# Performance work log

Measured on AMD Instinct MI355X. Metric: run time of the kernel, lower is better.

Reference implementation:

```python
import jax, jax.numpy as jnp
import numpy as np

N = 100000      # nodes
E = 1600000     # edges (before self loops)
H = 64          # hidden channels (per-head out dim, concat=False)
HEADS = 2
L = 2           # num GAT blocks
IN = 64
OUT = 10
B = 64          # graphs in batch
SLOPE = 0.2     # LeakyReLU negative slope (GATv2Conv default)
EPS = 1e-5      # BatchNorm eps


def setup_inputs() -> dict:
    key = jax.random.key(0)
    ks = jax.random.split(key, 10)
    s = 0.05
    x = jax.random.normal(ks[0], (N, IN), jnp.float32)
    edge_index = jax.random.randint(ks[1], (2, E), 0, N, dtype=jnp.int64)
    batch = jnp.sort(jax.random.randint(ks[2], (N,), 0, B, dtype=jnp.int64))
    W_enc = jax.random.normal(ks[3], (IN, H), jnp.float32) * s
    b_enc = jnp.zeros((H,), jnp.float32)
    Wl = jax.random.normal(ks[4], (L, H, HEADS * H), jnp.float32) * s
    bl = jnp.zeros((L, HEADS * H), jnp.float32)
    Wr = jax.random.normal(ks[5], (L, H, HEADS * H), jnp.float32) * s
    br = jnp.zeros((L, HEADS * H), jnp.float32)
    att = jax.random.normal(ks[6], (L, HEADS, H), jnp.float32) * s
    bias = jnp.zeros((L, H), jnp.float32)
    gamma = jnp.ones((L, H), jnp.float32)
    beta = jnp.zeros((L, H), jnp.float32)
    W_cls = jax.random.normal(ks[7], (H, OUT), jnp.float32) * s
    b_cls = jnp.zeros((OUT,), jnp.float32)
    return dict(x=x, edge_index=edge_index, batch=batch, W_enc=W_enc, b_enc=b_enc,
                Wl=Wl, bl=bl, Wr=Wr, br=br, att=att, bias=bias,
                gamma=gamma, beta=beta, W_cls=W_cls, b_cls=b_cls)


def reference(x, edge_index, batch, W_enc, b_enc, Wl, bl, Wr, br, att, bias,
              gamma, beta, W_cls, b_cls):
    # add self loops (GATv2Conv default add_self_loops=True)
    loops = jnp.arange(N, dtype=edge_index.dtype)
    ei = jnp.concatenate([edge_index, jnp.stack([loops, loops])], axis=1)
    src, dst = ei[0], ei[1]

    h = x @ W_enc + b_enc                                   # [N, H] atom encoder (Linear)
    for l in range(L):
        xl = (h @ Wl[l] + bl[l]).reshape(N, HEADS, H)       # source transform
        xr = (h @ Wr[l] + br[l]).reshape(N, HEADS, H)       # target transform
        # GATv2: e_uv = a^T LeakyReLU(W_l x_u + W_r x_v)
        z = jax.nn.leaky_relu(xl[src] + xr[dst], SLOPE)     # [E', heads, H]
        e = jnp.einsum('ehc,hc->eh', z, att[l])             # [E', heads]
        # segment softmax over incoming edges of each dst node
        m = jax.ops.segment_max(e, dst, num_segments=N)     # [N, heads]
        ex = jnp.exp(e - m[dst])
        den = jax.ops.segment_sum(ex, dst, num_segments=N)
        alpha = ex / den[dst]                               # [E', heads]
        out = jax.ops.segment_sum(xl[src] * alpha[:, :, None], dst, num_segments=N)
        h_new = out.mean(axis=1) + bias[l]                  # concat=False: mean over heads
        # BatchNorm1d (batch statistics) -> ReLU; dropout=0
        mu = h_new.mean(axis=0)
        var = h_new.var(axis=0)
        h = jax.nn.relu((h_new - mu) * jax.lax.rsqrt(var + EPS) * gamma[l] + beta[l])

    # global mean pool over graphs
    cnt = jax.ops.segment_sum(jnp.ones((N,), h.dtype), batch, num_segments=B)
    g = jax.ops.segment_sum(h, batch, num_segments=B) / jnp.maximum(cnt, 1.0)[:, None]
    return g @ W_cls + b_cls                                # [B, OUT]
```

## Files before the change

### kernel.cpp

```cpp
#include <hip/hip_runtime.h>

#define N_NODES 100000
#define E_EDGES 1600000
#define EP_EDGES (E_EDGES + N_NODES)
#define SLOPE 0.2f
#define BN_EPS 1e-5f
#define NB 8
#define NODES_PER_B 12500
#define NREP 32
#define SUBREG 8192
#define SCATTER_BLKS ((EP_EDGES + 255) / 256)

typedef _Float16 h2 __attribute__((ext_vector_type(2)));

#if defined(__has_builtin)
#if __has_builtin(__builtin_amdgcn_fdot2)
#define HAVE_FDOT2 1
#endif
#endif

__device__ __forceinline__ float fdot2f(h2 a, h2 b, float c) {
#ifdef HAVE_FDOT2
    return __builtin_amdgcn_fdot2(a, b, c, false);
#else
    return c + (float)a[0] * (float)b[0] + (float)a[1] * (float)b[1];
#endif
}
__device__ __forceinline__ h2 bch2(unsigned u) { return __builtin_bit_cast(h2, u); }
__device__ __forceinline__ h2 habs2(h2 z) {
    return __builtin_bit_cast(h2, (unsigned)(__builtin_bit_cast(unsigned, z) & 0x7fff7fffu));
}
__device__ __forceinline__ h2 shflx_h2(h2 a, int o) {
    return __builtin_bit_cast(h2, __shfl_xor(__builtin_bit_cast(int, a), o, 64));
}

template <int CTRL>
__device__ __forceinline__ float dpp_add_step(float v) {
    int r = __builtin_amdgcn_update_dpp(0, __float_as_int(v), CTRL, 0xF, 0xF, false);
    return v + __int_as_float(r);
}
__device__ __forceinline__ float rowsum16(float v) {
    v = dpp_add_step<0x128>(v);
    v = dpp_add_step<0x124>(v);
    v = dpp_add_step<0x122>(v);
    v = dpp_add_step<0x121>(v);
    return v;
}

__device__ __forceinline__ void bucket_scatter_body(int bid, const int* __restrict__ src,
                                                    const int* __restrict__ dst,
                                                    int* __restrict__ gcur, unsigned* __restrict__ ebuf) {
    int i = bid * 256 + threadIdx.x;
    int rep = bid & (NREP - 1);
    bool active = i < EP_EDGES;
    int s = 0, d = 0;
    if (i < E_EDGES) { s = src[i]; d = dst[i]; }
    else if (active) { s = i - E_EDGES; d = s; }
    int b = active ? (int)((unsigned)d / NODES_PER_B) : NB;
    unsigned long long lt = (1ull << (threadIdx.x & 63)) - 1ull;
    int rank = 0;
    unsigned long long mymask = 0;
#pragma unroll
    for (int bb = 0; bb < NB; ++bb) {
        unsigned long long m = __ballot(b == bb);
        if (b == bb) { rank = __popcll(m & lt); mymask = m; }
    }
    int leader = mymask ? (__ffsll((long long)mymask) - 1) : 0;
    int lanebit = threadIdx.x & 63;
    int chunkbase = 0;
    if (active && lanebit == leader)
        chunkbase = atomicAdd(&gcur[rep * NB + b], (int)__popcll(mymask));
    chunkbase = __shfl(chunkbase, leader, 64);
    if (active) {
        unsigned dl = (unsigned)d - (unsigned)b * NODES_PER_B;
        ebuf[(size_t)(rep * NB + b) * SUBREG + chunkbase + rank] = (dl << 17) | (unsigned)s;
    }
}

__device__ __forceinline__ void fuse_enc_body(const float* __restrict__ We, const float* __restrict__ be,
                                              const float* __restrict__ Wl, const float* __restrict__ bl,
                                              const float* __restrict__ Wr, const float* __restrict__ br,
                                              float* __restrict__ Wcl, float* __restrict__ bcl,
                                              float* __restrict__ Wcr, float* __restrict__ bcr,
                                              float (*sWe)[64], float* sbe) {
    int t = threadIdx.x;
    for (int i = t; i < 4096; i += 256) sWe[i & 63][i >> 6] = We[i];
    if (t < 64) sbe[t] = be[t];
    __syncthreads();
    int j = t & 127, side = t >> 7;
    const float* W  = side ? Wr : Wl;
    const float* bb = side ? br : bl;
    float acc[64];
#pragma unroll
    for (int k = 0; k < 64; ++k) acc[k] = 0.f;
    float bacc = bb[j];
    for (int m = 0; m < 64; ++m) {
        float wv = W[m * 128 + j];
        bacc += sbe[m] * wv;
#pragma unroll
        for (int k = 0; k < 64; ++k) acc[k] += sWe[m][k] * wv;
    }
    float* Wc = side ? Wcr : Wcl;
#pragma unroll
    for (int k = 0; k < 64; ++k) Wc[k * 128 + j] = acc[k];
    (side ? bcr : bcl)[j] = bacc;
}

__global__ __launch_bounds__(256) void scatter_fuse(const int* __restrict__ src, const int* __restrict__ dst,
                                                    int* __restrict__ gcur, unsigned* __restrict__ ebuf,
                                                    const float* __restrict__ We, const float* __restrict__ be,
                                                    const float* __restrict__ Wl, const float* __restrict__ bl,
                                                    const float* __restrict__ Wr, const float* __restrict__ br,
                                                    float* __restrict__ Wcl, float* __restrict__ bcl,
                                                    float* __restrict__ Wcr, float* __restrict__ bcr) {
    __shared__ float sWe[64][64];
    __shared__ float sbe[64];
    if (blockIdx.x == 0)
        fuse_enc_body(We, be, Wl, bl, Wr, br, Wcl, bcl, Wcr, bcr, sWe, sbe);
    else
        bucket_scatter_body(blockIdx.x - 1, src, dst, gcur, ebuf);
}

__global__ __launch_bounds__(256) void bucket_deg(const int* __restrict__ gcur,
                                                  const unsigned* __restrict__ ebuf,
                                                  int* __restrict__ deg) {
    __shared__ int ldeg[NODES_PER_B];
    int b = blockIdx.x & (NB - 1), rep = blockIdx.x >> 3;
    for (int j = threadIdx.x; j < NODES_PER_B; j += 256) ldeg[j] = 0;
    __syncthreads();
    int cnt = gcur[rep * NB + b];
    int base = b * NODES_PER_B;
    const unsigned* p = ebuf + (size_t)(rep * NB + b) * SUBREG;
    for (int i = threadIdx.x; i < cnt; i += 256)
        atomicAdd(&ldeg[p[i] >> 17], 1);
    __syncthreads();
    for (int j = threadIdx.x; j < NODES_PER_B; j += 256) {
        int v = ldeg[j];
        if (v) atomicAdd(&deg[base + j], v);
    }
}

__device__ __forceinline__ void bucket_fine_body(int bid, const int* __restrict__ gcur,
                                                 const unsigned* __restrict__ ebuf,
                                                 int* __restrict__ cursor, int* __restrict__ col) {
    int b = bid & (NB - 1), rep = bid >> 3;
    int cnt = gcur[rep * NB + b];
    int base = b * NODES_PER_B;
    const unsigned* p = ebuf + (size_t)(rep * NB + b) * SUBREG;
    for (int i = threadIdx.x; i < cnt; i += 256) {
        unsigned e = p[i];
        int d = base + (int)(e >> 17), s = (int)(e & 0x1FFFFu);
        int pos = atomicAdd(&cursor[d], 1);
        col[pos] = s;
    }
}

__global__ void scan_a(const int* __restrict__ deg, int* __restrict__ row_ptr, int* __restrict__ bsum) {
    __shared__ int wsum[16];
    int tid = threadIdx.x;
    int lane = tid & 63;
    int i = blockIdx.x * 1024 + tid;
    int x = (i < N_NODES) ? deg[i] : 0;
#pragma unroll
    for (int o = 1; o < 64; o <<= 1) {
        int y = __shfl_up(x, o, 64);
        if (lane >= o) x += y;
    }
    if (lane == 63) wsum[tid >> 6] = x;
    __syncthreads();
    if (tid < 16) {
        int s = wsum[tid];
#pragma unroll
        for (int o = 1; o < 16; o <<= 1) {
            int y = __shfl_up(s, o, 16);
            if (tid >= o) s += y;
        }
        wsum[tid] = s;
    }
    __syncthreads();
    int pre = (tid >= 64) ? wsum[(tid >> 6) - 1] : 0;
    int incl = x + pre;
    if (i < N_NODES) row_ptr[i + 1] = incl;
    if (tid == 1023) bsum[blockIdx.x] = incl;
}

__global__ void scan_c(int* __restrict__ cursor, int* __restrict__ row_ptr, const int* __restrict__ bsum) {
    __shared__ int sp[128];
    int t = threadIdx.x;
    if (t < 128) sp[t] = (t < 98) ? bsum[t] : 0;
    __syncthreads();
    for (int o = 1; o < 128; o <<= 1) {
        int v = (t < 128 && t >= o) ? sp[t - o] : 0;
        __syncthreads();
        if (t < 128) sp[t] += v;
        __syncthreads();
    }
    int i = blockIdx.x * 256 + t;
    if (i < N_NODES) {
        int d = cursor[i];
        int blk = i >> 10;
        int pre = blk ? sp[blk - 1] : 0;
        int incl = row_ptr[i + 1] + pre;
        row_ptr[i + 1] = incl;
        cursor[i] = incl - d;
        if (i == 0) row_ptr[0] = 0;
    }
}

template <int BN>
__device__ __forceinline__ void layer_gemm_body(int bid, int nb,
                                                const float* __restrict__ hin,
                                                const float* __restrict__ Wl, const float* __restrict__ bl,
                                                const float* __restrict__ Wr, const float* __restrict__ br,
                                                const float* __restrict__ bns, const float* __restrict__ gamma,
                                                const float* __restrict__ beta,
                                                unsigned short* __restrict__ xl, unsigned short* __restrict__ xr,
                                                float* ssc, float* ssh, h2 (*sh)[36]) {
    int t = threadIdx.x;
    if (BN) {
        if (t < 64) {
            float s = 0.f, sq = 0.f;
#pragma unroll
            for (int r = 0; r < 8; ++r) { s += bns[r * 128 + t]; sq += bns[r * 128 + 64 + t]; }
            float mu = s * (1.f / N_NODES);
            float var = sq * (1.f / N_NODES) - mu * mu;
            float sc = gamma[t] * rsqrtf(var + BN_EPS);
            ssc[t] = sc; ssh[t] = beta[t] - mu * sc;
        }
        __syncthreads();
    }
    int p = t & 127, rh = t >> 7;
    int col0 = 2 * p;
    bool isR = col0 >= 128;
    int cw0 = col0 & 127, cw1 = cw0 + 1;
    const float* W = isR ? Wr : Wl;
    h2 w2a[32], w2b[32];
#pragma unroll
    for (int k2 = 0; k2 < 32; ++k2) {
        w2a[k2] = (h2){(_Float16)W[(2 * k2) * 128 + cw0], (_Float16)W[(2 * k2 + 1) * 128 + cw0]};
        w2b[k2] = (h2){(_Float16)W[(2 * k2) * 128 + cw1], (_Float16)W[(2 * k2 + 1) * 128 + cw1]};
    }
    float bja = (isR ? br : bl)[cw0];
    float bjb = (isR ? br : bl)[cw1];
    int head0 = cw0 >> 6, c0 = cw0 & 63;
    int head1 = cw1 >> 6, c1 = cw1 & 63;
    int oidx0 = ((c0 >> 2) << 3) + (head0 << 2) + (c0 & 3);
    int oidx1 = ((c1 >> 2) << 3) + (head1 << 2) + (c1 & 3);
    unsigned short* dstp = isR ? xr : xl;
    for (int base = bid * 16; base < N_NODES; base += nb * 16) {
        __syncthreads();
#pragma unroll
        for (int pass = 0; pass < 2; ++pass) {
            int i = t + pass * 256;
            int node = i >> 5, pr = i & 31;
            int gnode = base + node;
            int cc = pr * 2;
            float2 v = make_float2(0.f, 0.f);
            if (gnode < N_NODES) v = *(const float2*)(hin + (size_t)gnode * 64 + cc);
            if (BN) {
                v.x = fmaxf(v.x * ssc[cc] + ssh[cc], 0.f);
                v.y = fmaxf(v.y * ssc[cc + 1] + ssh[cc + 1], 0.f);
            }
            sh[node][pr] = (h2){(_Float16)v.x, (_Float16)v.y};
        }
        __syncthreads();
        int lim = min(16, N_NODES - base);
        int rend = min(rh * 8 + 8, lim);
        for (int r = rh * 8; r < rend; ++r) {
            float acca = bja, accb = bjb;
            const uint4* r4 = (const uint4*)(&sh[r][0]);
#pragma unroll
            for (int k4 = 0; k4 < 8; ++k4) {
                uint4 u = r4[k4];
                acca = fdot2f(bch2(u.x), w2a[4 * k4 + 0], acca);
                accb = fdot2f(bch2(u.x), w2b[4 * k4 + 0], accb);
                acca = fdot2f(bch2(u.y), w2a[4 * k4 + 1], acca);
                accb = fdot2f(bch2(u.y), w2b[4 * k4 + 1], accb);
                acca = fdot2f(bch2(u.z), w2a[4 * k4 + 2], acca);
                accb = fdot2f(bch2(u.z), w2b[4 * k4 + 2], accb);
                acca = fdot2f(bch2(u.w), w2a[4 * k4 + 3], acca);
                accb = fdot2f(bch2(u.w), w2b[4 * k4 + 3], accb);
            }
            size_t rowb = (size_t)(base + r) * 128;
            dstp[rowb + oidx0] = __builtin_bit_cast(unsigned short, (_Float16)acca);
            dstp[rowb + oidx1] = __builtin_bit_cast(unsigned short, (_Float16)accb);
        }
    }
}

__global__ __launch_bounds__(256) void fine_gemm0(const int* __restrict__ gcur,
                                                  const unsigned* __restrict__ ebuf,
                                                  int* __restrict__ cursor, int* __restrict__ col,
                                                  const float* __restrict__ hin,
                                                  const float* __restrict__ Wl, const float* __restrict__ bl,
                                                  const float* __restrict__ Wr, const float* __restrict__ br,
                                                  unsigned short* __restrict__ xl, unsigned short* __restrict__ xr) {
    __shared__ float ssc[64], ssh[64];
    __shared__ h2 sh[16][36];
    if (blockIdx.x < NREP * NB)
        bucket_fine_body(blockIdx.x, gcur, ebuf, cursor, col);
    else
        layer_gemm_body<0>(blockIdx.x - NREP * NB, 1024, hin, Wl, bl, Wr, br,
                           nullptr, nullptr, nullptr, xl, xr, ssc, ssh, sh);
}

__global__ __launch_bounds__(256) void layer_gemm1(const float* __restrict__ hin,
                                                   const float* __restrict__ Wl, const float* __restrict__ bl,
                                                   const float* __restrict__ Wr, const float* __restrict__ br,
                                                   const float* __restrict__ bns, const float* __restrict__ gamma,
                                                   const float* __restrict__ beta,
                                                   unsigned short* __restrict__ xl, unsigned short* __restrict__ xr) {
    __shared__ float ssc[64], ssh[64];
    __shared__ h2 sh[16][36];
    layer_gemm_body<1>(blockIdx.x, gridDim.x, hin, Wl, bl, Wr, br, bns, gamma, beta, xl, xr, ssc, ssh, sh);
}

__global__ __launch_bounds__(256) void aggregate(const char* __restrict__ xlb,
                                                 const uint4* __restrict__ xr4,
                                                 const int* __restrict__ row_ptr, const int* __restrict__ col,
                                                 const float* __restrict__ att_l, const float* __restrict__ bias_l,
                                                 float* __restrict__ hn, float* __restrict__ bnsum) {
    int lane = threadIdx.x & 63, wid = threadIdx.x >> 6;
    int q = lane >> 4, k = lane & 15;
    int koff = k << 4;
    h2 atA0 = {(_Float16)att_l[4 * k], (_Float16)att_l[4 * k + 1]};
    h2 atA1 = {(_Float16)att_l[4 * k + 2], (_Float16)att_l[4 * k + 3]};
    h2 atB0 = {(_Float16)att_l[64 + 4 * k], (_Float16)att_l[64 + 4 * k + 1]};
    h2 atB1 = {(_Float16)att_l[64 + 4 * k + 2], (_Float16)att_l[64 + 4 * k + 3]};
    float bi0 = bias_l[4 * k], bi1 = bias_l[4 * k + 1], bi2 = bias_l[4 * k + 2], bi3 = bias_l[4 * k + 3];
    const h2 c06 = {(_Float16)0.6f, (_Float16)0.6f};
    const h2 c04 = {(_Float16)0.4f, (_Float16)0.4f};
    float ps[4] = {0, 0, 0, 0}, pq[4] = {0, 0, 0, 0};
    int w = blockIdx.x * 4 + wid, nw = gridDim.x * 4;
    for (int v = w; v < N_NODES; v += nw) {
        uint4 rp = xr4[(size_t)v * 16 + k];
        h2 rA0 = bch2(rp.x), rA1 = bch2(rp.y), rB0 = bch2(rp.z), rB1 = bch2(rp.w);
        int beg = row_ptr[v], end = row_ptr[v + 1];
        float s0 = 0.f, s1 = 0.f;
        h2 aA0 = {0, 0}, aA1 = {0, 0}, aB0 = {0, 0}, aB1 = {0, 0};
        const int* cptr = col + beg + q;
        int cv0 = cptr[0], cv1 = cptr[4], cv2 = cptr[8], cv3 = cptr[12];
        cptr += 16;
        uint4 lp0 = *(const uint4*)(xlb + (((size_t)(unsigned)cv0) << 8) + koff);
        uint4 lp1 = lp0, lp2 = lp0;
        if (beg + 4 < end) lp1 = *(const uint4*)(xlb + (((size_t)(unsigned)cv1) << 8) + koff);
        if (beg + 8 < end) lp2 = *(const uint4*)(xlb + (((size_t)(unsigned)cv2) << 8) + koff);
#pragma unroll 2
        for (int i = beg; i < end; i += 4) {
            uint4 lp3 = lp2;
            if (i + 12 < end) lp3 = *(const uint4*)(xlb + (((size_t)(unsigned)cv3) << 8) + koff);
            cv3 = *cptr; cptr += 4;
            h2 lA0 = bch2(lp0.x), lA1 = bch2(lp0.y), lB0 = bch2(lp0.z), lB1 = bch2(lp0.w);
            h2 zA0 = lA0 + rA0, zA1 = lA1 + rA1, zB0 = lB0 + rB0, zB1 = lB1 + rB1;
            h2 yA0 = zA0 * c06 + habs2(zA0) * c04;
            h2 yA1 = zA1 * c06 + habs2(zA1) * c04;
            h2 yB0 = zB0 * c06 + habs2(zB0) * c04;
            h2 yB1 = zB1 * c06 + habs2(zB1) * c04;
            float t0 = fdot2f(yA1, atA1, fdot2f(yA0, atA0, 0.f));
            float t1 = fdot2f(yB1, atB1, fdot2f(yB0, atB0, 0.f));
            t0 = rowsum16(t0); t1 = rowsum16(t1);
            bool valid = (i + q) < end;
            float p0 = valid ? __expf(t0) : 0.f;
            float p1 = valid ? __expf(t1) : 0.f;
            s0 += p0; s1 += p1;
            h2 p0h = {(_Float16)p0, (_Float16)p0};
            h2 p1h = {(_Float16)p1, (_Float16)p1};
            aA0 += p0h * lA0; aA1 += p0h * lA1;
            aB0 += p1h * lB0; aB1 += p1h * lB1;
            lp0 = lp1; lp1 = lp2; lp2 = lp3;
        }
#pragma unroll
        for (int o = 16; o <= 32; o <<= 1) {
            s0 += __shfl_xor(s0, o, 64); s1 += __shfl_xor(s1, o, 64);
            aA0 += shflx_h2(aA0, o); aA1 += shflx_h2(aA1, o);
            aB0 += shflx_h2(aB0, o); aB1 += shflx_h2(aB1, o);
        }
        if (q == 0) {
            float i0 = 0.5f / s0, i1 = 0.5f / s1;
            float hv0 = (float)aA0[0] * i0 + (float)aB0[0] * i1 + bi0;
            float hv1 = (float)aA0[1] * i0 + (float)aB0[1] * i1 + bi1;
            float hv2 = (float)aA1[0] * i0 + (float)aB1[0] * i1 + bi2;
            float hv3 = (float)aA1[1] * i0 + (float)aB1[1] * i1 + bi3;
            *(float4*)(hn + (size_t)v * 64 + 4 * k) = make_float4(hv0, hv1, hv2, hv3);
            ps[0] += hv0; pq[0] += hv0 * hv0;
            ps[1] += hv1; pq[1] += hv1 * hv1;
            ps[2] += hv2; pq[2] += hv2 * hv2;
            ps[3] += hv3; pq[3] += hv3 * hv3;
        }
    }
    __shared__ float sb[2][4][64];
    if (q == 0) {
#pragma unroll
        for (int j = 0; j < 4; ++j) { sb[0][wid][4 * k + j] = ps[j]; sb[1][wid][4 * k + j] = pq[j]; }
    }
    __syncthreads();
    float* dstb = bnsum + (size_t)(blockIdx.x & 7) * 128;
    int t = threadIdx.x;
    if (t < 64)
        atomicAdd(&dstb[t], sb[0][0][t] + sb[0][1][t] + sb[0][2][t] + sb[0][3][t]);
    else if (t < 128)
        atomicAdd(&dstb[t], sb[1][0][t - 64] + sb[1][1][t - 64] + sb[1][2][t - 64] + sb[1][3][t - 64]);
}

__global__ __launch_bounds__(256) void pool2(const float* __restrict__ hn, const int* __restrict__ batch,
                                             const float* __restrict__ bns, const float* __restrict__ gamma,
                                             const float* __restrict__ beta,
                                             float* __restrict__ gpool, float* __restrict__ gcnt) {
    __shared__ float ssc[64], ssh[64];
    int t = threadIdx.x;
    if (t < 64) {
        float s = 0.f, sq = 0.f;
#pragma unroll
        for (int r = 0; r < 8; ++r) { s += bns[r * 128 + t]; sq += bns[r * 128 + 64 + t]; }
        float mu = s * (1.f / N_NODES);
        float var = sq * (1.f / N_NODES) - mu * mu;
        float sc = gamma[t] * rsqrtf(var + BN_EPS);
        ssc[t] = sc; ssh[t] = beta[t] - mu * sc;
    }
    __syncthreads();
    int g = blockIdx.x >> 2, part = blockIdx.x & 3;
    int lo = 0, hi = N_NODES;
    while (lo < hi) { int mid = (lo + hi) >> 1; if (batch[mid] < g) lo = mid + 1; else hi = mid; }
    int lo2 = lo, hi2 = N_NODES;
    while (lo2 < hi2) { int mid = (lo2 + hi2) >> 1; if (batch[mid] < g + 1) lo2 = mid + 1; else hi2 = mid; }
    int len = lo2 - lo;
    if (part == 0 && t == 0) gcnt[g] = (float)len;
    int n0 = lo + (len * part) / 4, n1 = lo + (len * (part + 1)) / 4;
    int c = t & 63, r = t >> 6;
    float sc = ssc[c], sh = ssh[c];
    float acc = 0.f;
    for (int node = n0 + r; node < n1; node += 4)
        acc += fmaxf(hn[(size_t)node * 64 + c] * sc + sh, 0.f);
    __shared__ float sb[4][64];
    sb[r][c] = acc;
    __syncthreads();
    if (r == 0)
        atomicAdd(&gpool[g * 64 + c], sb[0][c] + sb[1][c] + sb[2][c] + sb[3][c]);
}

__global__ void classify(const float* __restrict__ gpool, const float* __restrict__ gcnt,
                         const float* __restrict__ Wc, const float* __restrict__ bc, float* __restrict__ out) {
    int t = threadIdx.x;
    if (t >= 640) return;
    int b = t / 10, o = t % 10;
    float inv = 1.f / fmaxf(gcnt[b], 1.f);
    float acc = 0.f;
    for (int c = 0; c < 64; ++c) acc += gpool[b * 64 + c] * Wc[c * 10 + o];
    out[t] = acc * inv + bc[o];
}

extern "C" void kernel_launch(void* const* d_in, const int* in_sizes, int n_in,
                              void* d_out, int out_size, void* d_ws, size_t ws_size,
                              hipStream_t stream) {
    (void)in_sizes; (void)n_in; (void)out_size; (void)ws_size;
    const float* x     = (const float*)d_in[0];
    const int*   ei    = (const int*)d_in[1];
    const int*   batch = (const int*)d_in[2];
    const float* W_enc = (const float*)d_in[3];
    const float* b_enc = (const float*)d_in[4];
    const float* Wl    = (const float*)d_in[5];
    const float* bl    = (const float*)d_in[6];
    const float* Wr    = (const float*)d_in[7];
    const float* br    = (const float*)d_in[8];
    const float* att   = (const float*)d_in[9];
    const float* bias  = (const float*)d_in[10];
    const float* gamma = (const float*)d_in[11];
    const float* beta  = (const float*)d_in[12];
    const float* Wc    = (const float*)d_in[13];
    const float* bc    = (const float*)d_in[14];
    float* out = (float*)d_out;

    char* ws = (char*)d_ws;
    size_t off = 0;
    auto A = [&](size_t bytes) { size_t r = off; off += (bytes + 255) & ~(size_t)255; return r; };

    int* row_ptr = (int*)(ws + A((N_NODES + 1) * 4));
    size_t colv_off = A((size_t)EP_EDGES * 4 + 426240);
    int* colv = (int*)(ws + colv_off);
    char* zbase = ws + colv_off + (size_t)EP_EDGES * 4;
    int*   cursor = (int*)(zbase + 128);
    int*   gcur   = (int*)(zbase + 400128);
    float* bns    = (float*)(zbase + 401152);
    float* gpool  = (float*)(zbase + 409344);
    float* gcnt   = (float*)(zbase + 425728);
    const size_t ZBYTES = 426240;

    float* h   = (float*)(ws + A((size_t)N_NODES * 64 * 4));
    float* hn  = (float*)(ws + A((size_t)N_NODES * 64 * 4));
    unsigned short* xl = (unsigned short*)(ws + A((size_t)N_NODES * 128 * 2));
    unsigned short* xr = (unsigned short*)(ws + A((size_t)N_NODES * 128 * 2));
    unsigned* ebuf = (unsigned*)(ws + A((size_t)NREP * NB * SUBREG * 4));
    int* bsum  = (int*)(ws + A(512));
    float* Wcl = (float*)(ws + A(64 * 128 * 4));
    float* Wcr = (float*)(ws + A(64 * 128 * 4));
    float* bcl = (float*)(ws + A(128 * 4));
    float* bcr = (float*)(ws + A(128 * 4));

    const int* srcv = ei;
    const int* dstv = ei + E_EDGES;

    hipMemsetAsync(zbase, 0, ZBYTES, stream);

    scatter_fuse<<<SCATTER_BLKS + 1, 256, 0, stream>>>(srcv, dstv, gcur, ebuf,
                                                       W_enc, b_enc, Wl, bl, Wr, br,
                                                       Wcl, bcl, Wcr, bcr);
    bucket_deg<<<NREP * NB, 256, 0, stream>>>(gcur, ebuf, cursor);
    scan_a<<<98, 1024, 0, stream>>>(cursor, row_ptr, bsum);
    scan_c<<<(N_NODES + 255) / 256, 256, 0, stream>>>(cursor, row_ptr, bsum);

    fine_gemm0<<<NREP * NB + 1024, 256, 0, stream>>>(gcur, ebuf, cursor, colv,
                                                     x, Wcl, bcl, Wcr, bcr, xl, xr);
    aggregate<<<4096, 256, 0, stream>>>((const char*)xl, (const uint4*)xr,
                                        row_ptr, colv, att, bias, hn, bns);
    layer_gemm1<<<1024, 256, 0, stream>>>(hn, Wl + 64 * 128, bl + 128, Wr + 64 * 128, br + 128,
                                          bns, gamma, beta, xl, xr);
    aggregate<<<4096, 256, 0, stream>>>((const char*)xl, (const uint4*)xr,
                                        row_ptr, colv, att + 128, bias + 64, h, bns + 1024);

    pool2<<<256, 256, 0, stream>>>(h, batch, bns + 1024, gamma + 64, beta + 64, gpool, gcnt);
    classify<<<1, 640, 0, stream>>>(gpool, gcnt, Wc, bc, out);
}
```

Before: 422.0 us.

## Fuse degree count with layer-0 GEMM and interleave two nodes in aggregate

The layer-0 GEMM moves from the fine bucket-fill kernel into the degree-count kernel, and the bucket fill becomes its own kernel launched after the scans. The degree counter now packs two 16-bit counts per shared-memory word, halving its LDS footprint so more blocks fit per CU. The aggregate kernel processes two destination nodes per wavefront at once, interleaving their gather loops to expose more memory-level parallelism. In exchange, the node pair runs to the longer of the two neighbour lists, which wastes work on degree imbalance and uses more registers.

```diff
diff --git a/kernel.cpp b/kernel.cpp
--- a/kernel.cpp
+++ b/kernel.cpp
@@ -119,92 +119,6 @@
         fuse_enc_body(We, be, Wl, bl, Wr, br, Wcl, bcl, Wcr, bcr, sWe, sbe);
     else
         bucket_scatter_body(blockIdx.x - 1, src, dst, gcur, ebuf);
-}
-
-__global__ __launch_bounds__(256) void bucket_deg(const int* __restrict__ gcur,
-                                                  const unsigned* __restrict__ ebuf,
-                                                  int* __restrict__ deg) {
-    __shared__ int ldeg[NODES_PER_B];
-    int b = blockIdx.x & (NB - 1), rep = blockIdx.x >> 3;
-    for (int j = threadIdx.x; j < NODES_PER_B; j += 256) ldeg[j] = 0;
-    __syncthreads();
-    int cnt = gcur[rep * NB + b];
-    int base = b * NODES_PER_B;
-    const unsigned* p = ebuf + (size_t)(rep * NB + b) * SUBREG;
-    for (int i = threadIdx.x; i < cnt; i += 256)
-        atomicAdd(&ldeg[p[i] >> 17], 1);
-    __syncthreads();
-    for (int j = threadIdx.x; j < NODES_PER_B; j += 256) {
-        int v = ldeg[j];
-        if (v) atomicAdd(&deg[base + j], v);
-    }
-}
-
-__device__ __forceinline__ void bucket_fine_body(int bid, const int* __restrict__ gcur,
-                                                 const unsigned* __restrict__ ebuf,
-                                                 int* __restrict__ cursor, int* __restrict__ col) {
-    int b = bid & (NB - 1), rep = bid >> 3;
-    int cnt = gcur[rep * NB + b];
-    int base = b * NODES_PER_B;
-    const unsigned* p = ebuf + (size_t)(rep * NB + b) * SUBREG;
-    for (int i = threadIdx.x; i < cnt; i += 256) {
-        unsigned e = p[i];
-        int d = base + (int)(e >> 17), s = (int)(e & 0x1FFFFu);
-        int pos = atomicAdd(&cursor[d], 1);
-        col[pos] = s;
-    }
-}
-
-__global__ void scan_a(const int* __restrict__ deg, int* __restrict__ row_ptr, int* __restrict__ bsum) {
-    __shared__ int wsum[16];
-    int tid = threadIdx.x;
-    int lane = tid & 63;
-    int i = blockIdx.x * 1024 + tid;
-    int x = (i < N_NODES) ? deg[i] : 0;
-#pragma unroll
-    for (int o = 1; o < 64; o <<= 1) {
-        int y = __shfl_up(x, o, 64);
-        if (lane >= o) x += y;
-    }
-    if (lane == 63) wsum[tid >> 6] = x;
-    __syncthreads();
-    if (tid < 16) {
-        int s = wsum[tid];
-#pragma unroll
-        for (int o = 1; o < 16; o <<= 1) {
-            int y = __shfl_up(s, o, 16);
-            if (tid >= o) s += y;
-        }
-        wsum[tid] = s;
-    }
-    __syncthreads();
-    int pre = (tid >= 64) ? wsum[(tid >> 6) - 1] : 0;
-    int incl = x + pre;
-    if (i < N_NODES) row_ptr[i + 1] = incl;
-    if (tid == 1023) bsum[blockIdx.x] = incl;
-}
-
-__global__ void scan_c(int* __restrict__ cursor, int* __restrict__ row_ptr, const int* __restrict__ bsum) {
-    __shared__ int sp[128];
-    int t = threadIdx.x;
-    if (t < 128) sp[t] = (t < 98) ? bsum[t] : 0;
-    __syncthreads();
-    for (int o = 1; o < 128; o <<= 1) {
-        int v = (t < 128 && t >= o) ? sp[t - o] : 0;
-        __syncthreads();
-        if (t < 128) sp[t] += v;
-        __syncthreads();
-    }
-    int i = blockIdx.x * 256 + t;
-    if (i < N_NODES) {
-        int d = cursor[i];
-        int blk = i >> 10;
-        int pre = blk ? sp[blk - 1] : 0;
-        int incl = row_ptr[i + 1] + pre;
-        row_ptr[i + 1] = incl;
-        cursor[i] = incl - d;
-        if (i == 0) row_ptr[0] = 0;
-    }
 }
 
 template <int BN>
@@ -288,20 +202,103 @@
     }
 }
 
-__global__ __launch_bounds__(256) void fine_gemm0(const int* __restrict__ gcur,
-                                                  const unsigned* __restrict__ ebuf,
-                                                  int* __restrict__ cursor, int* __restrict__ col,
-                                                  const float* __restrict__ hin,
-                                                  const float* __restrict__ Wl, const float* __restrict__ bl,
-                                                  const float* __restrict__ Wr, const float* __restrict__ br,
-                                                  unsigned short* __restrict__ xl, unsigned short* __restrict__ xr) {
+__global__ __launch_bounds__(256) void deg_gemm0(const int* __restrict__ gcur,
+                                                 const unsigned* __restrict__ ebuf,
+                                                 int* __restrict__ deg,
+                                                 const float* __restrict__ hin,
+                                                 const float* __restrict__ Wl, const float* __restrict__ bl,
+                                                 const float* __restrict__ Wr, const float* __restrict__ br,
+                                                 unsigned short* __restrict__ xl, unsigned short* __restrict__ xr) {
+    __shared__ unsigned ldeg2[NODES_PER_B / 2];
     __shared__ float ssc[64], ssh[64];
     __shared__ h2 sh[16][36];
-    if (blockIdx.x < NREP * NB)
-        bucket_fine_body(blockIdx.x, gcur, ebuf, cursor, col);
-    else
+    if (blockIdx.x < NREP * NB) {
+        int b = blockIdx.x & (NB - 1), rep = blockIdx.x >> 3;
+        for (int j = threadIdx.x; j < NODES_PER_B / 2; j += 256) ldeg2[j] = 0;
+        __syncthreads();
+        int cnt = gcur[rep * NB + b];
+        int base = b * NODES_PER_B;
+        const unsigned* p = ebuf + (size_t)(rep * NB + b) * SUBREG;
+        for (int i = threadIdx.x; i < cnt; i += 256) {
+            unsigned dl = p[i] >> 17;
+            atomicAdd(&ldeg2[dl >> 1], 1u << ((dl & 1) * 16));
+        }
+        __syncthreads();
+        for (int j = threadIdx.x; j < NODES_PER_B; j += 256) {
+            unsigned v = (ldeg2[j >> 1] >> ((j & 1) * 16)) & 0xffffu;
+            if (v) atomicAdd(&deg[base + j], (int)v);
+        }
+    } else {
         layer_gemm_body<0>(blockIdx.x - NREP * NB, 1024, hin, Wl, bl, Wr, br,
                            nullptr, nullptr, nullptr, xl, xr, ssc, ssh, sh);
+    }
+}
+
+__global__ __launch_bounds__(256) void bucket_fine(const int* __restrict__ gcur,
+                                                   const unsigned* __restrict__ ebuf,
+                                                   int* __restrict__ cursor, int* __restrict__ col) {
+    int b = blockIdx.x & (NB - 1), rep = blockIdx.x >> 3;
+    int cnt = gcur[rep * NB + b];
+    int base = b * NODES_PER_B;
+    const unsigned* p = ebuf + (size_t)(rep * NB + b) * SUBREG;
+    for (int i = threadIdx.x; i < cnt; i += 256) {
+        unsigned e = p[i];
+        int d = base + (int)(e >> 17), s = (int)(e & 0x1FFFFu);
+        int pos = atomicAdd(&cursor[d], 1);
+        col[pos] = s;
+    }
+}
+
+__global__ void scan_a(const int* __restrict__ deg, int* __restrict__ row_ptr, int* __restrict__ bsum) {
+    __shared__ int wsum[16];
+    int tid = threadIdx.x;
+    int lane = tid & 63;
+    int i = blockIdx.x * 1024 + tid;
+    int x = (i < N_NODES) ? deg[i] : 0;
+#pragma unroll
+    for (int o = 1; o < 64; o <<= 1) {
+        int y = __shfl_up(x, o, 64);
+        if (lane >= o) x += y;
+    }
+    if (lane == 63) wsum[tid >> 6] = x;
+    __syncthreads();
+    if (tid < 16) {
+        int s = wsum[tid];
+#pragma unroll
+        for (int o = 1; o < 16; o <<= 1) {
+            int y = __shfl_up(s, o, 16);
+            if (tid >= o) s += y;
+        }
+        wsum[tid] = s;
+    }
+    __syncthreads();
+    int pre = (tid >= 64) ? wsum[(tid >> 6) - 1] : 0;
+    int incl = x + pre;
+    if (i < N_NODES) row_ptr[i + 1] = incl;
+    if (tid == 1023) bsum[blockIdx.x] = incl;
+}
+
+__global__ void scan_c(int* __restrict__ cursor, int* __restrict__ row_ptr, const int* __restrict__ bsum) {
+    __shared__ int sp[128];
+    int t = threadIdx.x;
+    if (t < 128) sp[t] = (t < 98) ? bsum[t] : 0;
+    __syncthreads();
+    for (int o = 1; o < 128; o <<= 1) {
+        int v = (t < 128 && t >= o) ? sp[t - o] : 0;
+        __syncthreads();
+        if (t < 128) sp[t] += v;
+        __syncthreads();
+    }
+    int i = blockIdx.x * 256 + t;
+    if (i < N_NODES) {
+        int d = cursor[i];
+        int blk = i >> 10;
+        int pre = blk ? sp[blk - 1] : 0;
+        int incl = row_ptr[i + 1] + pre;
+        row_ptr[i + 1] = incl;
+        cursor[i] = incl - d;
+        if (i == 0) row_ptr[0] = 0;
+    }
 }
 
 __global__ __launch_bounds__(256) void layer_gemm1(const float* __restrict__ hin,
@@ -332,60 +329,85 @@
     const h2 c04 = {(_Float16)0.4f, (_Float16)0.4f};
     float ps[4] = {0, 0, 0, 0}, pq[4] = {0, 0, 0, 0};
     int w = blockIdx.x * 4 + wid, nw = gridDim.x * 4;
-    for (int v = w; v < N_NODES; v += nw) {
-        uint4 rp = xr4[(size_t)v * 16 + k];
-        h2 rA0 = bch2(rp.x), rA1 = bch2(rp.y), rB0 = bch2(rp.z), rB1 = bch2(rp.w);
-        int beg = row_ptr[v], end = row_ptr[v + 1];
-        float s0 = 0.f, s1 = 0.f;
-        h2 aA0 = {0, 0}, aA1 = {0, 0}, aB0 = {0, 0}, aB1 = {0, 0};
-        const int* cptr = col + beg + q;
-        int cv0 = cptr[0], cv1 = cptr[4], cv2 = cptr[8], cv3 = cptr[12];
-        cptr += 16;
-        uint4 lp0 = *(const uint4*)(xlb + (((size_t)(unsigned)cv0) << 8) + koff);
-        uint4 lp1 = lp0, lp2 = lp0;
-        if (beg + 4 < end) lp1 = *(const uint4*)(xlb + (((size_t)(unsigned)cv1) << 8) + koff);
-        if (beg + 8 < end) lp2 = *(const uint4*)(xlb + (((size_t)(unsigned)cv2) << 8) + koff);
-#pragma unroll 2
-        for (int i = beg; i < end; i += 4) {
-            uint4 lp3 = lp2;
-            if (i + 12 < end) lp3 = *(const uint4*)(xlb + (((size_t)(unsigned)cv3) << 8) + koff);
-            cv3 = *cptr; cptr += 4;
-            h2 lA0 = bch2(lp0.x), lA1 = bch2(lp0.y), lB0 = bch2(lp0.z), lB1 = bch2(lp0.w);
-            h2 zA0 = lA0 + rA0, zA1 = lA1 + rA1, zB0 = lB0 + rB0, zB1 = lB1 + rB1;
-            h2 yA0 = zA0 * c06 + habs2(zA0) * c04;
-            h2 yA1 = zA1 * c06 + habs2(zA1) * c04;
-            h2 yB0 = zB0 * c06 + habs2(zB0) * c04;
-            h2 yB1 = zB1 * c06 + habs2(zB1) * c04;
-            float t0 = fdot2f(yA1, atA1, fdot2f(yA0, atA0, 0.f));
-            float t1 = fdot2f(yB1, atB1, fdot2f(yB0, atB0, 0.f));
-            t0 = rowsum16(t0); t1 = rowsum16(t1);
-            bool valid = (i + q) < end;
-            float p0 = valid ? __expf(t0) : 0.f;
-            float p1 = valid ? __expf(t1) : 0.f;
-            s0 += p0; s1 += p1;
-            h2 p0h = {(_Float16)p0, (_Float16)p0};
-            h2 p1h = {(_Float16)p1, (_Float16)p1};
-            aA0 += p0h * lA0; aA1 += p0h * lA1;
-            aB0 += p1h * lB0; aB1 += p1h * lB1;
-            lp0 = lp1; lp1 = lp2; lp2 = lp3;
-        }
-#pragma unroll
-        for (int o = 16; o <= 32; o <<= 1) {
-            s0 += __shfl_xor(s0, o, 64); s1 += __shfl_xor(s1, o, 64);
-            aA0 += shflx_h2(aA0, o); aA1 += shflx_h2(aA1, o);
-            aB0 += shflx_h2(aB0, o); aB1 += shflx_h2(aB1, o);
-        }
-        if (q == 0) {
-            float i0 = 0.5f / s0, i1 = 0.5f / s1;
-            float hv0 = (float)aA0[0] * i0 + (float)aB0[0] * i1 + bi0;
-            float hv1 = (float)aA0[1] * i0 + (float)aB0[1] * i1 + bi1;
-            float hv2 = (float)aA1[0] * i0 + (float)aB1[0] * i1 + bi2;
-            float hv3 = (float)aA1[1] * i0 + (float)aB1[1] * i1 + bi3;
-            *(float4*)(hn + (size_t)v * 64 + 4 * k) = make_float4(hv0, hv1, hv2, hv3);
-            ps[0] += hv0; pq[0] += hv0 * hv0;
-            ps[1] += hv1; pq[1] += hv1 * hv1;
-            ps[2] += hv2; pq[2] += hv2 * hv2;
-            ps[3] += hv3; pq[3] += hv3 * hv3;
+    for (int vb = w; vb < N_NODES; vb += 2 * nw) {
+        bool has1 = (vb + nw) < N_NODES;
+        int va[2]; va[0] = vb; va[1] = has1 ? vb + nw : vb;
+        h2 rA0[2], rA1[2], rB0[2], rB1[2];
+        int len[2];
+        const int* cptr[2];
+        int cv2[2], cv3[2];
+        uint4 lp0[2], lp1[2];
+        float s0[2] = {0.f, 0.f}, s1[2] = {0.f, 0.f};
+        h2 aA0[2] = {{0, 0}, {0, 0}}, aA1[2] = {{0, 0}, {0, 0}};
+        h2 aB0[2] = {{0, 0}, {0, 0}}, aB1[2] = {{0, 0}, {0, 0}};
+#pragma unroll
+        for (int u = 0; u < 2; ++u) {
+            uint4 rp = xr4[(size_t)va[u] * 16 + k];
+            rA0[u] = bch2(rp.x); rA1[u] = bch2(rp.y); rB0[u] = bch2(rp.z); rB1[u] = bch2(rp.w);
+            int b = row_ptr[va[u]], e = row_ptr[va[u] + 1];
+            int l = (u == 1 && !has1) ? 0 : (e - b);
+            len[u] = l;
+            cptr[u] = col + b + q;
+            int c0 = cptr[u][0], c1 = cptr[u][4];
+            cv2[u] = cptr[u][8]; cv3[u] = cptr[u][12];
+            cptr[u] += 16;
+            lp0[u] = *(const uint4*)(xlb + (((size_t)(unsigned)c0) << 8) + koff);
+            lp1[u] = lp0[u];
+            if (4 < l) lp1[u] = *(const uint4*)(xlb + (((size_t)(unsigned)c1) << 8) + koff);
+        }
+        int n = max(len[0], len[1]);
+        for (int j = 0; j < n; j += 4) {
+#pragma unroll
+            for (int u = 0; u < 2; ++u) {
+                uint4 lp2 = lp1[u];
+                if (j + 8 < len[u])
+                    lp2 = *(const uint4*)(xlb + (((size_t)(unsigned)cv2[u]) << 8) + koff);
+                cv2[u] = cv3[u];
+                cv3[u] = *cptr[u]; cptr[u] += 4;
+                h2 lA0 = bch2(lp0[u].x), lA1 = bch2(lp0[u].y), lB0 = bch2(lp0[u].z), lB1 = bch2(lp0[u].w);
+                h2 zA0 = lA0 + rA0[u], zA1 = lA1 + rA1[u], zB0 = lB0 + rB0[u], zB1 = lB1 + rB1[u];
+                h2 yA0 = zA0 * c06 + habs2(zA0) * c04;
+                h2 yA1 = zA1 * c06 + habs2(zA1) * c04;
+                h2 yB0 = zB0 * c06 + habs2(zB0) * c04;
+                h2 yB1 = zB1 * c06 + habs2(zB1) * c04;
+                float t0 = fdot2f(yA1, atA1, fdot2f(yA0, atA0, 0.f));
+                float t1 = fdot2f(yB1, atB1, fdot2f(yB0, atB0, 0.f));
+                t0 = rowsum16(t0); t1 = rowsum16(t1);
+                bool valid = (j + q) < len[u];
+                float p0 = valid ? __expf(t0) : 0.f;
+                float p1 = valid ? __expf(t1) : 0.f;
+                s0[u] += p0; s1[u] += p1;
+                h2 p0h = {(_Float16)p0, (_Float16)p0};
+                h2 p1h = {(_Float16)p1, (_Float16)p1};
+                aA0[u] += p0h * lA0; aA1[u] += p0h * lA1;
+                aB0[u] += p1h * lB0; aB1[u] += p1h * lB1;
+                lp0[u] = lp1[u]; lp1[u] = lp2;
+            }
+        }
+#pragma unroll
+        for (int u = 0; u < 2; ++u) {
+            if (u == 0 || has1) {
+                float S0 = s0[u], S1 = s1[u];
+                h2 A0 = aA0[u], A1 = aA1[u], B0 = aB0[u], B1 = aB1[u];
+#pragma unroll
+                for (int o = 16; o <= 32; o <<= 1) {
+                    S0 += __shfl_xor(S0, o, 64); S1 += __shfl_xor(S1, o, 64);
+                    A0 += shflx_h2(A0, o); A1 += shflx_h2(A1, o);
+                    B0 += shflx_h2(B0, o); B1 += shflx_h2(B1, o);
+                }
+                if (q == 0) {
+                    float i0 = 0.5f / S0, i1 = 0.5f / S1;
+                    float hv0 = (float)A0[0] * i0 + (float)B0[0] * i1 + bi0;
+                    float hv1 = (float)A0[1] * i0 + (float)B0[1] * i1 + bi1;
+                    float hv2 = (float)A1[0] * i0 + (float)B1[0] * i1 + bi2;
+                    float hv3 = (float)A1[1] * i0 + (float)B1[1] * i1 + bi3;
+                    *(float4*)(hn + (size_t)va[u] * 64 + 4 * k) = make_float4(hv0, hv1, hv2, hv3);
+                    ps[0] += hv0; pq[0] += hv0 * hv0;
+                    ps[1] += hv1; pq[1] += hv1 * hv1;
+                    ps[2] += hv2; pq[2] += hv2 * hv2;
+                    ps[3] += hv3; pq[3] += hv3 * hv3;
+                }
+            }
         }
     }
     __shared__ float sb[2][4][64];
@@ -504,12 +526,12 @@
     scatter_fuse<<<SCATTER_BLKS + 1, 256, 0, stream>>>(srcv, dstv, gcur, ebuf,
                                                        W_enc, b_enc, Wl, bl, Wr, br,
                                                        Wcl, bcl, Wcr, bcr);
-    bucket_deg<<<NREP * NB, 256, 0, stream>>>(gcur, ebuf, cursor);
+    deg_gemm0<<<NREP * NB + 1024, 256, 0, stream>>>(gcur, ebuf, cursor,
+                                                    x, Wcl, bcl, Wcr, bcr, xl, xr);
     scan_a<<<98, 1024, 0, stream>>>(cursor, row_ptr, bsum);
     scan_c<<<(N_NODES + 255) / 256, 256, 0, stream>>>(cursor, row_ptr, bsum);
-
-    fine_gemm0<<<NREP * NB + 1024, 256, 0, stream>>>(gcur, ebuf, cursor, colv,
-                                                     x, Wcl, bcl, Wcr, bcr, xl, xr);
+    bucket_fine<<<NREP * NB, 256, 0, stream>>>(gcur, ebuf, cursor, colv);
+
     aggregate<<<4096, 256, 0, stream>>>((const char*)xl, (const uint4*)xr,
                                         row_ptr, colv, att, bias, hn, bns);
     layer_gemm1<<<1024, 256, 0, stream>>>(hn, Wl + 64 * 128, bl + 128, Wr + 64 * 128, br + 128,
```

Measured after the change: 495.2 us. +17.4%, slower.
